# Kernel optimization log

Hardware: AMD Instinct MI355X
Metric: run time of the kernel (lower is better)

## Reference

```python
import jax, jax.numpy as jnp
import numpy as np

NUM_LINKS = 1048576


def _euler_rots(theta):
    # theta: [N,3] -> per-link rotation R = Rz @ Ry @ Rx, shape [N,3,3]
    cx, cy, cz = jnp.cos(theta[:, 0]), jnp.cos(theta[:, 1]), jnp.cos(theta[:, 2])
    sx, sy, sz = jnp.sin(theta[:, 0]), jnp.sin(theta[:, 1]), jnp.sin(theta[:, 2])
    z = jnp.zeros_like(cx)
    o = jnp.ones_like(cx)
    rx = jnp.stack([jnp.stack([o, z, z], -1),
                    jnp.stack([z, cx, -sx], -1),
                    jnp.stack([z, sx, cx], -1)], -2)
    ry = jnp.stack([jnp.stack([cy, z, sy], -1),
                    jnp.stack([z, o, z], -1),
                    jnp.stack([-sy, z, cy], -1)], -2)
    rz = jnp.stack([jnp.stack([cz, -sz, z], -1),
                    jnp.stack([sz, cz, z], -1),
                    jnp.stack([z, z, o], -1)], -2)
    return jnp.matmul(rz, jnp.matmul(ry, rx))  # [N,3,3]


def setup_inputs() -> dict:
    key = jax.random.key(0)
    k1, k2 = jax.random.split(key)
    link_lengths = jax.random.uniform(k1, (NUM_LINKS,), dtype=jnp.float32)
    theta = jax.random.normal(k2, (NUM_LINKS, 3), dtype=jnp.float32)
    return {"link_lengths": link_lengths, "theta": theta}


def reference(link_lengths, theta):
    # Original loop computes eff_pos_i = sum_{j=0..i} (R_0 @ R_1 @ ... @ R_j) @ t_j
    # with t_j = l_j * e_z. Vectorize via prefix matrix products + cumsum.
    R = _euler_rots(theta)                                   # [N,3,3]
    P = jax.lax.associative_scan(jnp.matmul, R)              # P_j = R_0@...@R_j
    v = P[:, :, 2] * link_lengths[:, None]                   # P_j @ (l_j * e_z)
    return jnp.cumsum(v, axis=0)                             # [N,3]
```

## Files before the change

### kernel.cpp

```cpp
#include <hip/hip_runtime.h>
#include <math.h>


#define TPB 256
#define EPT 4
#define EPB (TPB * EPT)
#define MAXB 1024
#define NWAVE (TPB / 64)

struct Xf {
    float m[9];
    float p[3];
};

__device__ __forceinline__ void xf_identity(Xf& x) {
    x.m[0] = 1.f; x.m[1] = 0.f; x.m[2] = 0.f;
    x.m[3] = 0.f; x.m[4] = 1.f; x.m[5] = 0.f;
    x.m[6] = 0.f; x.m[7] = 0.f; x.m[8] = 1.f;
    x.p[0] = 0.f; x.p[1] = 0.f; x.p[2] = 0.f;
}

__device__ __forceinline__ Xf xf_comb(const Xf& A, const Xf& B) {
    Xf o;
#pragma unroll
    for (int r = 0; r < 3; ++r) {
        const float a0 = A.m[r * 3 + 0], a1 = A.m[r * 3 + 1], a2 = A.m[r * 3 + 2];
#pragma unroll
        for (int c = 0; c < 3; ++c) {
            o.m[r * 3 + c] = a0 * B.m[0 * 3 + c] + a1 * B.m[1 * 3 + c] + a2 * B.m[2 * 3 + c];
        }
        o.p[r] = A.p[r] + a0 * B.p[0] + a1 * B.p[1] + a2 * B.p[2];
    }
    return o;
}

__device__ __forceinline__ void xf_fold(Xf& a, float ax, float ay, float az, float l) {
    float sx, cx, sy, cy, sz, cz;
    sincosf(ax, &sx, &cx);
    sincosf(ay, &sy, &cy);
    sincosf(az, &sz, &cz);
    const float sysx = sy * sx, sycx = sy * cx;
    const float r00 = cz * cy;
    const float r01 = cz * sysx - sz * cx;
    const float r02 = sz * sx + cz * sycx;
    const float r10 = sz * cy;
    const float r11 = cz * cx + sz * sysx;
    const float r12 = sz * sycx - cz * sx;
    const float r20 = -sy;
    const float r21 = cy * sx;
    const float r22 = cy * cx;
    const float t0 = l * r02, t1 = l * r12, t2 = l * r22;
    const float p0 = a.p[0] + a.m[0] * t0 + a.m[1] * t1 + a.m[2] * t2;
    const float p1 = a.p[1] + a.m[3] * t0 + a.m[4] * t1 + a.m[5] * t2;
    const float p2 = a.p[2] + a.m[6] * t0 + a.m[7] * t1 + a.m[8] * t2;
    const float n0 = a.m[0] * r00 + a.m[1] * r10 + a.m[2] * r20;
    const float n1 = a.m[0] * r01 + a.m[1] * r11 + a.m[2] * r21;
    const float n2 = a.m[0] * r02 + a.m[1] * r12 + a.m[2] * r22;
    const float n3 = a.m[3] * r00 + a.m[4] * r10 + a.m[5] * r20;
    const float n4 = a.m[3] * r01 + a.m[4] * r11 + a.m[5] * r21;
    const float n5 = a.m[3] * r02 + a.m[4] * r12 + a.m[5] * r22;
    const float n6 = a.m[6] * r00 + a.m[7] * r10 + a.m[8] * r20;
    const float n7 = a.m[6] * r01 + a.m[7] * r11 + a.m[8] * r21;
    const float n8 = a.m[6] * r02 + a.m[7] * r12 + a.m[8] * r22;
    a.m[0] = n0; a.m[1] = n1; a.m[2] = n2;
    a.m[3] = n3; a.m[4] = n4; a.m[5] = n5;
    a.m[6] = n6; a.m[7] = n7; a.m[8] = n8;
    a.p[0] = p0; a.p[1] = p1; a.p[2] = p2;
}

__device__ __forceinline__ Xf xf_shfl_up(const Xf& a, int delta) {
    Xf o;
#pragma unroll
    for (int k = 0; k < 9; ++k) o.m[k] = __shfl_up(a.m[k], delta, 64);
#pragma unroll
    for (int k = 0; k < 3; ++k) o.p[k] = __shfl_up(a.p[k], delta, 64);
    return o;
}

__device__ __forceinline__ Xf wave_scan(Xf a, int lane) {
#pragma unroll
    for (int off = 1; off < 64; off <<= 1) {
        const Xf b = xf_shfl_up(a, off);
        if (lane >= off) a = xf_comb(b, a);
    }
    return a;
}

__device__ __forceinline__ Xf xf_load4(const Xf* p) {
    const float4* g = (const float4*)p;
    const float4 x = g[0], y = g[1], z = g[2];
    Xf b;
    b.m[0] = x.x; b.m[1] = x.y; b.m[2] = x.z;
    b.m[3] = x.w; b.m[4] = y.x; b.m[5] = y.y;
    b.m[6] = y.z; b.m[7] = y.w; b.m[8] = z.x;
    b.p[0] = z.y; b.p[1] = z.z; b.p[2] = z.w;
    return b;
}
__device__ __forceinline__ void xf_store4(Xf* p, const Xf& b) {
    float4* g = (float4*)p;
    g[0] = make_float4(b.m[0], b.m[1], b.m[2], b.m[3]);
    g[1] = make_float4(b.m[4], b.m[5], b.m[6], b.m[7]);
    g[2] = make_float4(b.m[8], b.p[0], b.p[1], b.p[2]);
}

__device__ __forceinline__ void local_fold(const float* __restrict__ ll,
                                           const float* __restrict__ th,
                                           long long j0, int n, Xf& a,
                                           float pe[EPT][3]) {
    xf_identity(a);
    if (j0 + EPT <= n) {
        const float4* th4 = (const float4*)(th + 3 * j0);
        const float4 A = th4[0], B = th4[1], C = th4[2];
        const float4 L = *(const float4*)(ll + j0);
        xf_fold(a, A.x, A.y, A.z, L.x);
        pe[0][0] = a.p[0]; pe[0][1] = a.p[1]; pe[0][2] = a.p[2];
        xf_fold(a, A.w, B.x, B.y, L.y);
        pe[1][0] = a.p[0]; pe[1][1] = a.p[1]; pe[1][2] = a.p[2];
        xf_fold(a, B.z, B.w, C.x, L.z);
        pe[2][0] = a.p[0]; pe[2][1] = a.p[1]; pe[2][2] = a.p[2];
        xf_fold(a, C.y, C.z, C.w, L.w);
        pe[3][0] = a.p[0]; pe[3][1] = a.p[1]; pe[3][2] = a.p[2];
    } else {
#pragma unroll
        for (int e = 0; e < EPT; ++e) {
            const long long j = j0 + e;
            if (j < n) xf_fold(a, th[3 * j + 0], th[3 * j + 1], th[3 * j + 2], ll[j]);
            pe[e][0] = a.p[0]; pe[e][1] = a.p[1]; pe[e][2] = a.p[2];
        }
    }
}

__device__ __forceinline__ void write_out(float* __restrict__ out, long long j0, int n,
                                          const Xf& T, const float pe[EPT][3]) {
    if (j0 + EPT <= n) {
        float o[EPT * 3];
#pragma unroll
        for (int e = 0; e < EPT; ++e) {
            const float q0 = pe[e][0], q1 = pe[e][1], q2 = pe[e][2];
            o[e * 3 + 0] = T.p[0] + T.m[0] * q0 + T.m[1] * q1 + T.m[2] * q2;
            o[e * 3 + 1] = T.p[1] + T.m[3] * q0 + T.m[4] * q1 + T.m[5] * q2;
            o[e * 3 + 2] = T.p[2] + T.m[6] * q0 + T.m[7] * q1 + T.m[8] * q2;
        }
        float4* o4 = (float4*)(out + 3 * j0);
        o4[0] = make_float4(o[0], o[1], o[2], o[3]);
        o4[1] = make_float4(o[4], o[5], o[6], o[7]);
        o4[2] = make_float4(o[8], o[9], o[10], o[11]);
    } else {
#pragma unroll
        for (int e = 0; e < EPT; ++e) {
            const long long j = j0 + e;
            if (j < n) {
                const float q0 = pe[e][0], q1 = pe[e][1], q2 = pe[e][2];
                out[3 * j + 0] = T.p[0] + T.m[0] * q0 + T.m[1] * q1 + T.m[2] * q2;
                out[3 * j + 1] = T.p[1] + T.m[3] * q0 + T.m[4] * q1 + T.m[5] * q2;
                out[3 * j + 2] = T.p[2] + T.m[6] * q0 + T.m[7] * q1 + T.m[8] * q2;
            }
        }
    }
}

__global__ void __launch_bounds__(TPB) fk_phase1(const float* __restrict__ ll,
                                                 const float* __restrict__ th,
                                                 Xf* __restrict__ agg, int n) {
    __shared__ Xf wagg[NWAVE];
    const int t = threadIdx.x;
    const int lane = t & 63, w = t >> 6;
    const long long j0 = (long long)blockIdx.x * EPB + (long long)t * EPT;

    Xf a;
    float pe[EPT][3];
    local_fold(ll, th, j0, n, a, pe);

    const Xf inc = wave_scan(a, lane);
    if (lane == 63) wagg[w] = inc;
    __syncthreads();

    if (t == TPB - 1) {
        Xf acc = wagg[0];
#pragma unroll
        for (int k = 1; k < NWAVE - 1; ++k) acc = xf_comb(acc, wagg[k]);
        acc = xf_comb(acc, inc);
        xf_store4(&agg[blockIdx.x], acc);
    }
}

__global__ void __launch_bounds__(TPB) fk_phase2(const Xf* __restrict__ agg,
                                                 Xf* __restrict__ pfx, int nb) {
    __shared__ Xf wagg[NWAVE];
    const int t = threadIdx.x;
    const int lane = t & 63, w = t >> 6;
    const int i0 = t * EPT;

    Xf q[EPT];
    Xf a;
    xf_identity(a);
#pragma unroll
    for (int e = 0; e < EPT; ++e) {
        const int i = i0 + e;
        if (i < nb) a = xf_comb(a, xf_load4(&agg[i]));
        q[e] = a;
    }

    const Xf inc = wave_scan(a, lane);
    if (lane == 63) wagg[w] = inc;
    __syncthreads();

    Xf exw;
    xf_identity(exw);
    for (int k = 0; k < w; ++k) exw = xf_comb(exw, wagg[k]);

    Xf ext = xf_shfl_up(inc, 1);
    Xf T;
    if (lane == 0) T = exw;
    else T = xf_comb(exw, ext);

    if (i0 < nb) xf_store4(&pfx[i0], T);
#pragma unroll
    for (int e = 1; e < EPT; ++e) {
        if (i0 + e < nb) {
            Xf v = xf_comb(T, q[e - 1]);
            xf_store4(&pfx[i0 + e], v);
        }
    }
}

__global__ void __launch_bounds__(TPB) fk_phase3(const float* __restrict__ ll,
                                                 const float* __restrict__ th,
                                                 const Xf* __restrict__ pfx,
                                                 float* __restrict__ out, int n) {
    __shared__ Xf wagg[NWAVE];
    const int t = threadIdx.x;
    const int lane = t & 63, w = t >> 6;
    const long long j0 = (long long)blockIdx.x * EPB + (long long)t * EPT;

    Xf a;
    float pe[EPT][3];
    local_fold(ll, th, j0, n, a, pe);

    const Xf inc = wave_scan(a, lane);
    if (lane == 63) wagg[w] = inc;
    __syncthreads();

    Xf exw;
    xf_identity(exw);
    for (int k = 0; k < w; ++k) exw = xf_comb(exw, wagg[k]);

    const Xf ext = xf_shfl_up(inc, 1);

    const Xf G = xf_load4(&pfx[blockIdx.x]);
    Xf T = xf_comb(G, exw);
    if (lane != 0) T = xf_comb(T, ext);

    write_out(out, j0, n, T, pe);
}

extern "C" void kernel_launch(void* const* d_in, const int* in_sizes, int n_in,
                              void* d_out, int out_size, void* d_ws, size_t ws_size,
                              hipStream_t stream) {
    const float* ll = (const float*)d_in[0];
    const float* th = (const float*)d_in[1];
    float* out = (float*)d_out;
    const int n = in_sizes[0];

    int nb = (n + EPB - 1) / EPB;
    if (nb > MAXB) nb = MAXB;

    Xf* agg = (Xf*)d_ws;
    Xf* pfx = agg + MAXB;

    fk_phase1<<<nb, TPB, 0, stream>>>(ll, th, agg, n);
    fk_phase2<<<1, TPB, 0, stream>>>(agg, pfx, nb);
    fk_phase3<<<nb, TPB, 0, stream>>>(ll, th, pfx, out, n);
}
```

Measured before the change: 32.30 us.

## Replace three-phase scan with single-pass flag-based lookback kernel

Merges the three kernels (block aggregate, aggregate scan, final fix-up) into one kernel. Each block publishes its aggregate with a release flag, and wave 0 then gathers all earlier block aggregates through acquire-polling and a wave reduction. This removes two kernel launches and the second pass that recomputed the per-link rotations and local fold. In exchange it adds a memset launch, a serial wait on predecessor blocks, and an O(bid/64) reduction per block. It also depends on earlier blocks being scheduled first so the spin-wait cannot deadlock.

```diff
diff --git a/kernel.cpp b/kernel.cpp
--- a/kernel.cpp
+++ b/kernel.cpp
@@ -76,6 +76,22 @@
     for (int k = 0; k < 3; ++k) o.p[k] = __shfl_up(a.p[k], delta, 64);
     return o;
 }
+__device__ __forceinline__ Xf xf_shfl_down(const Xf& a, int delta) {
+    Xf o;
+#pragma unroll
+    for (int k = 0; k < 9; ++k) o.m[k] = __shfl_down(a.m[k], delta, 64);
+#pragma unroll
+    for (int k = 0; k < 3; ++k) o.p[k] = __shfl_down(a.p[k], delta, 64);
+    return o;
+}
+__device__ __forceinline__ Xf xf_bcast0(const Xf& a) {
+    Xf o;
+#pragma unroll
+    for (int k = 0; k < 9; ++k) o.m[k] = __shfl(a.m[k], 0, 64);
+#pragma unroll
+    for (int k = 0; k < 3; ++k) o.p[k] = __shfl(a.p[k], 0, 64);
+    return o;
+}
 
 __device__ __forceinline__ Xf wave_scan(Xf a, int lane) {
 #pragma unroll
@@ -159,18 +175,19 @@
     }
 }
 
-__global__ void __launch_bounds__(TPB) fk_phase1(const float* __restrict__ ll,
-                                                 const float* __restrict__ th,
-                                                 Xf* __restrict__ agg, int n) {
+__global__ void __launch_bounds__(TPB, 4)
+fk_lookback(const float* __restrict__ ll, const float* __restrict__ th,
+            Xf* __restrict__ agg, unsigned* __restrict__ flags,
+            float* __restrict__ out, int n) {
     __shared__ Xf wagg[NWAVE];
-    const int t = threadIdx.x;
+    __shared__ Xf shG;
+    const int t = threadIdx.x, bid = blockIdx.x;
     const int lane = t & 63, w = t >> 6;
-    const long long j0 = (long long)blockIdx.x * EPB + (long long)t * EPT;
+    const long long j0 = (long long)bid * EPB + (long long)t * EPT;
 
     Xf a;
     float pe[EPT][3];
     local_fold(ll, th, j0, n, a, pe);
-
     const Xf inc = wave_scan(a, lane);
     if (lane == 63) wagg[w] = inc;
     __syncthreads();
@@ -180,75 +197,59 @@
 #pragma unroll
         for (int k = 1; k < NWAVE - 1; ++k) acc = xf_comb(acc, wagg[k]);
         acc = xf_comb(acc, inc);
-        xf_store4(&agg[blockIdx.x], acc);
-    }
-}
-
-__global__ void __launch_bounds__(TPB) fk_phase2(const Xf* __restrict__ agg,
-                                                 Xf* __restrict__ pfx, int nb) {
-    __shared__ Xf wagg[NWAVE];
-    const int t = threadIdx.x;
-    const int lane = t & 63, w = t >> 6;
-    const int i0 = t * EPT;
-
-    Xf q[EPT];
-    Xf a;
-    xf_identity(a);
-#pragma unroll
-    for (int e = 0; e < EPT; ++e) {
-        const int i = i0 + e;
-        if (i < nb) a = xf_comb(a, xf_load4(&agg[i]));
-        q[e] = a;
-    }
-
-    const Xf inc = wave_scan(a, lane);
-    if (lane == 63) wagg[w] = inc;
+        xf_store4(&agg[bid], acc);
+        __threadfence();
+        __hip_atomic_store(&flags[bid], 1u, __ATOMIC_RELEASE, __HIP_MEMORY_SCOPE_AGENT);
+    }
+
+    if (w == 0) {
+        Xf G;
+        xf_identity(G);
+        const int fullw = bid >> 6, rem = bid & 63;
+        for (int win = 0; win < fullw; ++win) {
+            const int idx = (win << 6) + lane;
+            while (__hip_atomic_load(&flags[idx], __ATOMIC_ACQUIRE,
+                                     __HIP_MEMORY_SCOPE_AGENT) == 0u) {
+                __builtin_amdgcn_s_sleep(1);
+            }
+            Xf v = xf_load4(&agg[idx]);
+#pragma unroll
+            for (int off = 1; off < 64; off <<= 1) {
+                const Xf b = xf_shfl_down(v, off);
+                if (lane + off < 64) v = xf_comb(v, b);
+            }
+            G = xf_comb(G, xf_bcast0(v));
+        }
+        if (rem) {
+            const int idx = (fullw << 6) + lane;
+            Xf v;
+            if (lane < rem) {
+                while (__hip_atomic_load(&flags[idx], __ATOMIC_ACQUIRE,
+                                         __HIP_MEMORY_SCOPE_AGENT) == 0u) {
+                    __builtin_amdgcn_s_sleep(1);
+                }
+                v = xf_load4(&agg[idx]);
+            } else {
+                xf_identity(v);
+            }
+#pragma unroll
+            for (int off = 1; off < 64; off <<= 1) {
+                const Xf b = xf_shfl_down(v, off);
+                if (lane + off < 64) v = xf_comb(v, b);
+            }
+            G = xf_comb(G, xf_bcast0(v));
+        }
+        if (lane == 0) shG = G;
+    }
     __syncthreads();
 
     Xf exw;
     xf_identity(exw);
     for (int k = 0; k < w; ++k) exw = xf_comb(exw, wagg[k]);
 
-    Xf ext = xf_shfl_up(inc, 1);
-    Xf T;
-    if (lane == 0) T = exw;
-    else T = xf_comb(exw, ext);
-
-    if (i0 < nb) xf_store4(&pfx[i0], T);
-#pragma unroll
-    for (int e = 1; e < EPT; ++e) {
-        if (i0 + e < nb) {
-            Xf v = xf_comb(T, q[e - 1]);
-            xf_store4(&pfx[i0 + e], v);
-        }
-    }
-}
-
-__global__ void __launch_bounds__(TPB) fk_phase3(const float* __restrict__ ll,
-                                                 const float* __restrict__ th,
-                                                 const Xf* __restrict__ pfx,
-                                                 float* __restrict__ out, int n) {
-    __shared__ Xf wagg[NWAVE];
-    const int t = threadIdx.x;
-    const int lane = t & 63, w = t >> 6;
-    const long long j0 = (long long)blockIdx.x * EPB + (long long)t * EPT;
-
-    Xf a;
-    float pe[EPT][3];
-    local_fold(ll, th, j0, n, a, pe);
-
-    const Xf inc = wave_scan(a, lane);
-    if (lane == 63) wagg[w] = inc;
-    __syncthreads();
-
-    Xf exw;
-    xf_identity(exw);
-    for (int k = 0; k < w; ++k) exw = xf_comb(exw, wagg[k]);
-
     const Xf ext = xf_shfl_up(inc, 1);
 
-    const Xf G = xf_load4(&pfx[blockIdx.x]);
-    Xf T = xf_comb(G, exw);
+    Xf T = xf_comb(shG, exw);
     if (lane != 0) T = xf_comb(T, ext);
 
     write_out(out, j0, n, T, pe);
@@ -266,9 +267,8 @@
     if (nb > MAXB) nb = MAXB;
 
     Xf* agg = (Xf*)d_ws;
-    Xf* pfx = agg + MAXB;
-
-    fk_phase1<<<nb, TPB, 0, stream>>>(ll, th, agg, n);
-    fk_phase2<<<1, TPB, 0, stream>>>(agg, pfx, nb);
-    fk_phase3<<<nb, TPB, 0, stream>>>(ll, th, pfx, out, n);
-}
+    unsigned* flags = (unsigned*)((char*)d_ws + MAXB * sizeof(Xf));
+
+    hipMemsetAsync(flags, 0, nb * sizeof(unsigned), stream);
+    fk_lookback<<<nb, TPB, 0, stream>>>(ll, th, agg, flags, out, n);
+}
```

Result: slower. 127.9 us (+295.9%).

## Drop single-block prefix kernel; each block reduces preceding aggregates itself

Applied to the files above, without the earlier changes.

Removes the middle single-block scan kernel that turned block aggregates into prefixes. Instead, every apply block reduces all preceding block aggregates with a block-wide reduction before its own local scan. Phase one also switches from a full wave scan to a cheaper shuffle-down reduction. This saves one launch and a serialized tiny kernel. The cost is redundant reading and combining of up to 1024 aggregates in every block.

```diff
diff --git a/kernel.cpp b/kernel.cpp
--- a/kernel.cpp
+++ b/kernel.cpp
@@ -76,6 +76,14 @@
     for (int k = 0; k < 3; ++k) o.p[k] = __shfl_up(a.p[k], delta, 64);
     return o;
 }
+__device__ __forceinline__ Xf xf_shfl_down(const Xf& a, int delta) {
+    Xf o;
+#pragma unroll
+    for (int k = 0; k < 9; ++k) o.m[k] = __shfl_down(a.m[k], delta, 64);
+#pragma unroll
+    for (int k = 0; k < 3; ++k) o.p[k] = __shfl_down(a.p[k], delta, 64);
+    return o;
+}
 
 __device__ __forceinline__ Xf wave_scan(Xf a, int lane) {
 #pragma unroll
@@ -84,6 +92,15 @@
         if (lane >= off) a = xf_comb(b, a);
     }
     return a;
+}
+
+__device__ __forceinline__ Xf wave_reduce(Xf v, int lane) {
+#pragma unroll
+    for (int off = 1; off < 64; off <<= 1) {
+        const Xf b = xf_shfl_down(v, off);
+        if (lane + off < 64) v = xf_comb(v, b);
+    }
+    return v;
 }
 
 __device__ __forceinline__ Xf xf_load4(const Xf* p) {
@@ -159,9 +176,9 @@
     }
 }
 
-__global__ void __launch_bounds__(TPB) fk_phase1(const float* __restrict__ ll,
-                                                 const float* __restrict__ th,
-                                                 Xf* __restrict__ agg, int n) {
+__global__ void __launch_bounds__(TPB) fk_agg(const float* __restrict__ ll,
+                                              const float* __restrict__ th,
+                                              Xf* __restrict__ agg, int n) {
     __shared__ Xf wagg[NWAVE];
     const int t = threadIdx.x;
     const int lane = t & 63, w = t >> 6;
@@ -171,84 +188,64 @@
     float pe[EPT][3];
     local_fold(ll, th, j0, n, a, pe);
 
+    const Xf red = wave_reduce(a, lane);
+    if (lane == 0) wagg[w] = red;
+    __syncthreads();
+
+    if (t == 0) {
+        Xf acc = wagg[0];
+#pragma unroll
+        for (int k = 1; k < NWAVE; ++k) acc = xf_comb(acc, wagg[k]);
+        xf_store4(&agg[blockIdx.x], acc);
+    }
+}
+
+__global__ void __launch_bounds__(TPB) fk_apply(const float* __restrict__ ll,
+                                                const float* __restrict__ th,
+                                                const Xf* __restrict__ agg,
+                                                float* __restrict__ out, int n) {
+    __shared__ Xf wred[NWAVE];
+    __shared__ Xf wagg[NWAVE];
+    __shared__ Xf shG;
+    const int t = threadIdx.x, bid = blockIdx.x;
+    const int lane = t & 63, w = t >> 6;
+    const long long j0 = (long long)bid * EPB + (long long)t * EPT;
+
+    {
+        const int i0 = t * EPT;
+        Xf A;
+        xf_identity(A);
+#pragma unroll
+        for (int e = 0; e < EPT; ++e) {
+            const int i = i0 + e;
+            if (i < bid) A = xf_comb(A, xf_load4(&agg[i]));
+        }
+        const Xf red = wave_reduce(A, lane);
+        if (lane == 0) wred[w] = red;
+    }
+    __syncthreads();
+    if (t == 0) {
+        Xf G = wred[0];
+#pragma unroll
+        for (int k = 1; k < NWAVE; ++k) G = xf_comb(G, wred[k]);
+        shG = G;
+    }
+
+    Xf a;
+    float pe[EPT][3];
+    local_fold(ll, th, j0, n, a, pe);
+
     const Xf inc = wave_scan(a, lane);
     if (lane == 63) wagg[w] = inc;
     __syncthreads();
 
-    if (t == TPB - 1) {
-        Xf acc = wagg[0];
-#pragma unroll
-        for (int k = 1; k < NWAVE - 1; ++k) acc = xf_comb(acc, wagg[k]);
-        acc = xf_comb(acc, inc);
-        xf_store4(&agg[blockIdx.x], acc);
-    }
-}
-
-__global__ void __launch_bounds__(TPB) fk_phase2(const Xf* __restrict__ agg,
-                                                 Xf* __restrict__ pfx, int nb) {
-    __shared__ Xf wagg[NWAVE];
-    const int t = threadIdx.x;
-    const int lane = t & 63, w = t >> 6;
-    const int i0 = t * EPT;
-
-    Xf q[EPT];
-    Xf a;
-    xf_identity(a);
-#pragma unroll
-    for (int e = 0; e < EPT; ++e) {
-        const int i = i0 + e;
-        if (i < nb) a = xf_comb(a, xf_load4(&agg[i]));
-        q[e] = a;
-    }
-
-    const Xf inc = wave_scan(a, lane);
-    if (lane == 63) wagg[w] = inc;
-    __syncthreads();
-
     Xf exw;
     xf_identity(exw);
     for (int k = 0; k < w; ++k) exw = xf_comb(exw, wagg[k]);
 
-    Xf ext = xf_shfl_up(inc, 1);
-    Xf T;
-    if (lane == 0) T = exw;
-    else T = xf_comb(exw, ext);
-
-    if (i0 < nb) xf_store4(&pfx[i0], T);
-#pragma unroll
-    for (int e = 1; e < EPT; ++e) {
-        if (i0 + e < nb) {
-            Xf v = xf_comb(T, q[e - 1]);
-            xf_store4(&pfx[i0 + e], v);
-        }
-    }
-}
-
-__global__ void __launch_bounds__(TPB) fk_phase3(const float* __restrict__ ll,
-                                                 const float* __restrict__ th,
-                                                 const Xf* __restrict__ pfx,
-                                                 float* __restrict__ out, int n) {
-    __shared__ Xf wagg[NWAVE];
-    const int t = threadIdx.x;
-    const int lane = t & 63, w = t >> 6;
-    const long long j0 = (long long)blockIdx.x * EPB + (long long)t * EPT;
-
-    Xf a;
-    float pe[EPT][3];
-    local_fold(ll, th, j0, n, a, pe);
-
-    const Xf inc = wave_scan(a, lane);
-    if (lane == 63) wagg[w] = inc;
-    __syncthreads();
-
-    Xf exw;
-    xf_identity(exw);
-    for (int k = 0; k < w; ++k) exw = xf_comb(exw, wagg[k]);
-
     const Xf ext = xf_shfl_up(inc, 1);
 
-    const Xf G = xf_load4(&pfx[blockIdx.x]);
-    Xf T = xf_comb(G, exw);
+    Xf T = xf_comb(shG, exw);
     if (lane != 0) T = xf_comb(T, ext);
 
     write_out(out, j0, n, T, pe);
@@ -266,9 +263,7 @@
     if (nb > MAXB) nb = MAXB;
 
     Xf* agg = (Xf*)d_ws;
-    Xf* pfx = agg + MAXB;
-
-    fk_phase1<<<nb, TPB, 0, stream>>>(ll, th, agg, n);
-    fk_phase2<<<1, TPB, 0, stream>>>(agg, pfx, nb);
-    fk_phase3<<<nb, TPB, 0, stream>>>(ll, th, pfx, out, n);
-}
+
+    fk_agg<<<nb, TPB, 0, stream>>>(ll, th, agg, n);
+    fk_apply<<<nb, TPB, 0, stream>>>(ll, th, agg, out, n);
+}
```

After: 30.83 us. -4.6%, faster.
